# Kernel tuning notes

Hardware: AMD Instinct MI355X
Metric: run time of the kernel (lower is better)

Reference implementation:

```python
import jax, jax.numpy as jnp
import numpy as np

B, H, S, D = 1, 16, 4096, 64

def setup_inputs() -> dict:
    key = jax.random.key(0)
    k1, k2, k3 = jax.random.split(key, 3)
    query = jax.random.normal(k1, (B, H, S, D), dtype=jnp.float32)
    key_t = jax.random.normal(k2, (B, H, S, D), dtype=jnp.float32)
    value = jax.random.normal(k3, (B, H, S, D), dtype=jnp.float32)
    attn_mask = jnp.zeros((B, 1, S, S), dtype=jnp.float32)
    return {"query": query, "key": key_t, "value": value, "attn_mask": attn_mask}

def reference(query, key, value, attn_mask):
    d = query.shape[-1]
    # [B,H,S,S] = QK^T / sqrt(d) + mask
    scores = jnp.einsum("bhqd,bhkd->bhqk", query, key) / jnp.sqrt(jnp.float32(d))
    scores = scores + attn_mask
    probs = jax.nn.softmax(scores, axis=-1)
    # dropout_p = 0.0 -> identity
    out = jnp.einsum("bhqk,bhkd->bhqd", probs, value)
    return out
```

## Files before the change

kernel.cpp:

```cpp
#include <hip/hip_runtime.h>
#include <stdint.h>

#define LOG2E  1.44269504088896f
#define QSCALE (0.125f * LOG2E)

typedef float    f32x4_t  __attribute__((ext_vector_type(4)));
typedef float    f32x16_t __attribute__((ext_vector_type(16)));
typedef _Float16 f16x8_t  __attribute__((ext_vector_type(8)));
typedef _Float16 f16x2_t  __attribute__((ext_vector_type(2)));

#if __has_builtin(__builtin_amdgcn_exp2f)
#define EXP2F(x) __builtin_amdgcn_exp2f(x)
#else
#define EXP2F(x) exp2f(x)
#endif

__device__ __forceinline__ float rowsum2(f16x2_t p, float acc) {
#if __has_builtin(__builtin_amdgcn_fdot2)
  return __builtin_amdgcn_fdot2(p, (f16x2_t){(_Float16)1.0f, (_Float16)1.0f}, acc, false);
#else
  return acc + (float)p[0] + (float)p[1];
#endif
}

__global__ void mask_scan_kernel(const float* __restrict__ m, int* __restrict__ flag) {
  const float* p = m + (size_t)blockIdx.x * 8192 + (size_t)threadIdx.x * 4;
  unsigned acc = 0;
#pragma unroll
  for (int i = 0; i < 8; ++i) {
    f32x4_t v = *(const f32x4_t*)(p + (size_t)i * 1024);
    acc |= __float_as_uint(v[0]) | __float_as_uint(v[1]) |
           __float_as_uint(v[2]) | __float_as_uint(v[3]);
  }
  acc &= 0x7fffffffu;
  if (acc) atomicOr(flag, 1);
}

__global__ void convert_qk_kernel(const float* __restrict__ Q, const float* __restrict__ K,
                                  _Float16* __restrict__ Qh, _Float16* __restrict__ Kh) {
  const size_t idx = ((size_t)blockIdx.x * 256 + threadIdx.x) * 8;
  {
    f32x4_t a = *(const f32x4_t*)(Q + idx);
    f32x4_t b = *(const f32x4_t*)(Q + idx + 4);
    union { _Float16 h[8]; uint4 q; } U;
#pragma unroll
    for (int j = 0; j < 4; ++j) { U.h[j] = (_Float16)(a[j] * QSCALE); U.h[4 + j] = (_Float16)(b[j] * QSCALE); }
    *(uint4*)(Qh + idx) = U.q;
  }
  {
    f32x4_t a = *(const f32x4_t*)(K + idx);
    f32x4_t b = *(const f32x4_t*)(K + idx + 4);
    union { _Float16 h[8]; uint4 q; } U;
#pragma unroll
    for (int j = 0; j < 4; ++j) { U.h[j] = (_Float16)a[j]; U.h[4 + j] = (_Float16)b[j]; }
    *(uint4*)(Kh + idx) = U.q;
  }
}

__global__ void transpose_v_kernel(const float* __restrict__ V, _Float16* __restrict__ Vth) {
  __shared__ __align__(16) _Float16 T[64 * 72];
  const int tid  = threadIdx.x;
  const int head = blockIdx.x >> 6;
  const int st   = blockIdx.x & 63;
  const size_t hoff = (size_t)head * 4096 * 64;

  const int sl    = tid >> 2;
  const int fbase = (tid & 3) * 16;
  const float* src = V + hoff + (size_t)(st * 64 + sl) * 64 + fbase;
#pragma unroll
  for (int c = 0; c < 4; ++c) {
    f32x4_t a = *(const f32x4_t*)(src + c * 4);
#pragma unroll
    for (int j = 0; j < 4; ++j) T[(fbase + c * 4 + j) * 72 + sl] = (_Float16)a[j];
  }
  __syncthreads();
  const int feat = tid >> 2;
  const int sb   = (tid & 3) * 16;
  uint4 r0 = *(const uint4*)&T[feat * 72 + sb];
  uint4 r1 = *(const uint4*)&T[feat * 72 + sb + 8];
  _Float16* dst = Vth + hoff + (size_t)feat * 4096 + st * 64 + sb;
  *(uint4*)(dst)     = r0;
  *(uint4*)(dst + 8) = r1;
}

template <bool WS16>
__launch_bounds__(256, 2)
__global__ void sdpa_kernel(const float* __restrict__ Qg, const float* __restrict__ Kg,
                            const float* __restrict__ Vg, const float* __restrict__ Mg,
                            const _Float16* __restrict__ Qh, const _Float16* __restrict__ Kh,
                            const _Float16* __restrict__ Vth,
                            float* __restrict__ Og, const int* __restrict__ flag) {
  __shared__ __align__(16) _Float16 Ks[64 * 72];
  __shared__ __align__(16) _Float16 Vt[64 * 72];

  const int tid  = threadIdx.x;
  const int bid  = blockIdx.x;
  const int hh   = ((bid & 7) << 1) | ((bid >> 3) & 1);
  const int qt   = bid >> 4;
  const int w    = tid >> 6;
  const int lane = tid & 63;
  const int n    = lane & 31;
  const int h2   = lane >> 5;
  const int sig  = (n & 0x13) | ((n >> 1) & 4) | ((n << 1) & 8);
  const bool has_mask = (*flag) != 0;

  const size_t hoff = (size_t)hh * 4096 * 64;
  const int qcol = qt * 128 + w * 32 + n;

  f16x8_t qf[4];
  if (WS16) {
    const _Float16* qp = Qh + hoff + (size_t)qcol * 64 + 8 * h2;
#pragma unroll
    for (int kh = 0; kh < 4; ++kh) qf[kh] = *(const f16x8_t*)(qp + kh * 16);
  } else {
    const float* qp = Qg + hoff + (size_t)qcol * 64 + 8 * h2;
#pragma unroll
    for (int kh = 0; kh < 4; ++kh) {
      f32x4_t a = *(const f32x4_t*)(qp + kh * 16);
      f32x4_t b = *(const f32x4_t*)(qp + kh * 16 + 4);
      union { _Float16 h[8]; f16x8_t v; } U;
#pragma unroll
      for (int j = 0; j < 4; ++j) { U.h[j] = (_Float16)(a[j] * QSCALE); U.h[4 + j] = (_Float16)(b[j] * QSCALE); }
      qf[kh] = U.v;
    }
  }

  f32x16_t o0 = {0.f,0.f,0.f,0.f,0.f,0.f,0.f,0.f,0.f,0.f,0.f,0.f,0.f,0.f,0.f,0.f};
  f32x16_t o1 = o0;
  float lacc = 0.0f;

#pragma unroll 1
  for (int kt = 0; kt < 64; ++kt) {
    const int kbase = kt * 64;

    uint4 kk0, kk1, vv0, vv1;
    f32x4_t k0, k1, k2, k3;
    float vlo[8], vhi[8];
    if (WS16) {
      const _Float16* kp = Kh + hoff + (size_t)(kbase + (tid >> 2)) * 64 + (tid & 3) * 16;
      kk0 = *(const uint4*)(kp);
      kk1 = *(const uint4*)(kp + 8);
      const _Float16* vp = Vth + hoff + (size_t)(tid >> 2) * 4096 + kbase + (tid & 3) * 16;
      vv0 = *(const uint4*)(vp);
      vv1 = *(const uint4*)(vp + 8);
    } else {
      const float* kp = Kg + hoff + (size_t)(kbase + (tid >> 2)) * 64 + (tid & 3) * 16;
      k0 = *(const f32x4_t*)(kp + 0);
      k1 = *(const f32x4_t*)(kp + 4);
      k2 = *(const f32x4_t*)(kp + 8);
      k3 = *(const f32x4_t*)(kp + 12);
      const float* vp = Vg + hoff + (size_t)(kbase + (tid >> 5) * 8) * 64 + (tid & 31);
#pragma unroll
      for (int j = 0; j < 8; ++j) {
        vlo[j] = vp[(size_t)j * 64];
        vhi[j] = vp[(size_t)j * 64 + 32];
      }
    }

    f32x4_t mk[2][2][2];
    if (has_mask) {
      const float* mp = Mg + (size_t)qcol * 4096 + kbase + 8 * h2;
#pragma unroll
      for (int kb = 0; kb < 2; ++kb)
#pragma unroll
        for (int a = 0; a < 2; ++a)
#pragma unroll
          for (int b = 0; b < 2; ++b)
            mk[kb][a][b] = *(const f32x4_t*)(mp + kb * 32 + 16 * a + 4 * b);
    }

    __syncthreads();

    if (WS16) {
      *(uint4*)&Ks[(tid >> 2) * 72 + (tid & 3) * 16]     = kk0;
      *(uint4*)&Ks[(tid >> 2) * 72 + (tid & 3) * 16 + 8] = kk1;
      *(uint4*)&Vt[(tid >> 2) * 72 + (tid & 3) * 16]     = vv0;
      *(uint4*)&Vt[(tid >> 2) * 72 + (tid & 3) * 16 + 8] = vv1;
    } else {
      union { _Float16 h[8]; uint4 q; } A, B;
#pragma unroll
      for (int j = 0; j < 4; ++j) {
        A.h[j] = (_Float16)k0[j];  A.h[4 + j] = (_Float16)k1[j];
        B.h[j] = (_Float16)k2[j];  B.h[4 + j] = (_Float16)k3[j];
      }
      *(uint4*)&Ks[(tid >> 2) * 72 + (tid & 3) * 16]     = A.q;
      *(uint4*)&Ks[(tid >> 2) * 72 + (tid & 3) * 16 + 8] = B.q;
      union { _Float16 h[8]; uint4 q; } C, D;
#pragma unroll
      for (int j = 0; j < 8; ++j) { C.h[j] = (_Float16)vlo[j]; D.h[j] = (_Float16)vhi[j]; }
      *(uint4*)&Vt[(tid & 31) * 72 + (tid >> 5) * 8]        = C.q;
      *(uint4*)&Vt[((tid & 31) + 32) * 72 + (tid >> 5) * 8] = D.q;
    }

    __syncthreads();

#pragma unroll
    for (int kb = 0; kb < 2; ++kb) {
      f32x16_t acc = {0.f,0.f,0.f,0.f,0.f,0.f,0.f,0.f,0.f,0.f,0.f,0.f,0.f,0.f,0.f,0.f};
#pragma unroll
      for (int kh = 0; kh < 4; ++kh) {
        const f16x8_t ka = *(const f16x8_t*)&Ks[(kb * 32 + sig) * 72 + kh * 16 + 8 * h2];
        acc = __builtin_amdgcn_mfma_f32_32x32x16_f16(ka, qf[kh], acc, 0, 0, 0);
      }
#pragma unroll
      for (int a = 0; a < 2; ++a) {
        union { _Float16 h[8]; f16x8_t v; f16x2_t p2[4]; } F;
#pragma unroll
        for (int idx = 0; idx < 8; ++idx) {
          float x = acc[8 * a + idx];
          if (has_mask) x = __builtin_fmaf(mk[kb][a][idx >> 2][idx & 3], LOG2E, x);
          F.h[idx] = (_Float16)EXP2F(x);
        }
#pragma unroll
        for (int t = 0; t < 4; ++t) lacc = rowsum2(F.p2[t], lacc);
        const int f = kb * 2 + a;
        const f16x8_t v0 = *(const f16x8_t*)&Vt[n * 72 + f * 16 + 8 * h2];
        o0 = __builtin_amdgcn_mfma_f32_32x32x16_f16(F.v, v0, o0, 0, 0, 0);
        const f16x8_t v1 = *(const f16x8_t*)&Vt[(32 + n) * 72 + f * 16 + 8 * h2];
        o1 = __builtin_amdgcn_mfma_f32_32x32x16_f16(F.v, v1, o1, 0, 0, 0);
      }
    }
  }

  float lq = lacc + __shfl_xor(lacc, 32);
  float* op = Og + hoff;
#pragma unroll
  for (int r2 = 0; r2 < 4; ++r2) {
#pragma unroll
    for (int rr = 0; rr < 4; ++rr) {
      const int reg  = r2 * 4 + rr;
      const int qrow = rr + 8 * r2 + 4 * h2;
      float lr  = __shfl(lq, qrow);
      float inv = 1.0f / lr;
      const size_t row = (size_t)(qt * 128 + w * 32 + qrow) * 64;
      op[row + n]      = o0[reg] * inv;
      op[row + 32 + n] = o1[reg] * inv;
    }
  }
}

extern "C" void kernel_launch(void* const* d_in, const int* in_sizes, int n_in,
                              void* d_out, int out_size, void* d_ws, size_t ws_size,
                              hipStream_t stream) {
  const float* Q = (const float*)d_in[0];
  const float* K = (const float*)d_in[1];
  const float* V = (const float*)d_in[2];
  const float* M = (const float*)d_in[3];
  float* O = (float*)d_out;

  const size_t NELEM = (size_t)16 * 4096 * 64;
  const size_t need  = 256 + 3 * NELEM * sizeof(_Float16);
  int* flag = (int*)d_ws;

  hipMemsetAsync(flag, 0, sizeof(int), stream);
  mask_scan_kernel<<<2048, 256, 0, stream>>>(M, flag);

  if (ws_size >= need) {
    _Float16* Qh  = (_Float16*)((char*)d_ws + 256);
    _Float16* Kh  = Qh + NELEM;
    _Float16* Vth = Kh + NELEM;
    convert_qk_kernel<<<2048, 256, 0, stream>>>(Q, K, Qh, Kh);
    transpose_v_kernel<<<1024, 256, 0, stream>>>(V, Vth);
    sdpa_kernel<true><<<512, 256, 0, stream>>>(Q, K, V, M, Qh, Kh, Vth, O, flag);
  } else {
    sdpa_kernel<false><<<512, 256, 0, stream>>>(Q, K, V, M, nullptr, nullptr, nullptr, O, flag);
  }
}
```

Baseline: 234.3 us.

## Process 64 query rows per wave and prefetch next K/V tile in registers

```diff
diff --git a/kernel.cpp b/kernel.cpp
--- a/kernel.cpp
+++ b/kernel.cpp
@@ -83,13 +83,156 @@
   *(uint4*)(dst + 8) = r1;
 }
 
-template <bool WS16>
+__launch_bounds__(128, 2)
+__global__ void sdpa_kernel2(const _Float16* __restrict__ Qh, const _Float16* __restrict__ Kh,
+                             const _Float16* __restrict__ Vth, const float* __restrict__ Mg,
+                             float* __restrict__ Og, const int* __restrict__ flag) {
+  __shared__ __align__(16) _Float16 Ks[64 * 72];
+  __shared__ __align__(16) _Float16 Vt[64 * 72];
+
+  const int t    = threadIdx.x;
+  const int bid  = blockIdx.x;
+  const int hh   = ((bid & 7) << 1) | ((bid >> 3) & 1);
+  const int qt   = bid >> 4;
+  const int w    = t >> 6;
+  const int lane = t & 63;
+  const int n    = lane & 31;
+  const int h2   = lane >> 5;
+  const int sig  = (n & 0x13) | ((n >> 1) & 4) | ((n << 1) & 8);
+  const bool has_mask = (*flag) != 0;
+
+  const size_t hoff = (size_t)hh * 4096 * 64;
+  const int qb = qt * 128 + w * 64;
+
+  f16x8_t qf[2][4];
+#pragma unroll
+  for (int qh = 0; qh < 2; ++qh) {
+    const _Float16* qp = Qh + hoff + (size_t)(qb + qh * 32 + n) * 64 + 8 * h2;
+#pragma unroll
+    for (int kh = 0; kh < 4; ++kh) qf[qh][kh] = *(const f16x8_t*)(qp + kh * 16);
+  }
+
+  f32x16_t o00 = {0.f,0.f,0.f,0.f,0.f,0.f,0.f,0.f,0.f,0.f,0.f,0.f,0.f,0.f,0.f,0.f};
+  f32x16_t o01 = o00, o10 = o00, o11 = o00;
+  float lacc0 = 0.0f, lacc1 = 0.0f;
+
+  const int sr = t >> 1;
+  const int sh = (t & 1) * 32;
+  const _Float16* kbase_p = Kh  + hoff + (size_t)sr * 64 + sh;
+  const _Float16* vbase_p = Vth + hoff + (size_t)sr * 4096 + sh;
+
+  uint4 kk[4], vv[4];
+#pragma unroll
+  for (int j = 0; j < 4; ++j) {
+    kk[j] = ((const uint4*)kbase_p)[j];
+    vv[j] = ((const uint4*)vbase_p)[j];
+  }
+
+#pragma unroll 1
+  for (int kt = 0; kt < 64; ++kt) {
+    const int kbase = kt * 64;
+
+    __syncthreads();
+    {
+      uint4* kd = (uint4*)&Ks[sr * 72 + sh];
+      uint4* vd = (uint4*)&Vt[sr * 72 + sh];
+#pragma unroll
+      for (int j = 0; j < 4; ++j) { kd[j] = kk[j]; vd[j] = vv[j]; }
+    }
+    __syncthreads();
+
+    if (kt < 63) {
+      const _Float16* kp = kbase_p + (size_t)(kbase + 64) * 64;
+      const _Float16* vp = vbase_p + (kbase + 64);
+#pragma unroll
+      for (int j = 0; j < 4; ++j) {
+        kk[j] = ((const uint4*)kp)[j];
+        vv[j] = ((const uint4*)vp)[j];
+      }
+    }
+
+#pragma unroll
+    for (int kb = 0; kb < 2; ++kb) {
+      f16x8_t ka[4];
+#pragma unroll
+      for (int kh = 0; kh < 4; ++kh)
+        ka[kh] = *(const f16x8_t*)&Ks[(kb * 32 + sig) * 72 + kh * 16 + 8 * h2];
+      f32x16_t s0 = {0.f,0.f,0.f,0.f,0.f,0.f,0.f,0.f,0.f,0.f,0.f,0.f,0.f,0.f,0.f,0.f};
+      f32x16_t s1 = s0;
+#pragma unroll
+      for (int kh = 0; kh < 4; ++kh) {
+        s0 = __builtin_amdgcn_mfma_f32_32x32x16_f16(ka[kh], qf[0][kh], s0, 0, 0, 0);
+        s1 = __builtin_amdgcn_mfma_f32_32x32x16_f16(ka[kh], qf[1][kh], s1, 0, 0, 0);
+      }
+
+#pragma unroll
+      for (int a = 0; a < 2; ++a) {
+        const int f = kb * 2 + a;
+        const f16x8_t v0 = *(const f16x8_t*)&Vt[n * 72 + f * 16 + 8 * h2];
+        const f16x8_t v1 = *(const f16x8_t*)&Vt[(32 + n) * 72 + f * 16 + 8 * h2];
+#pragma unroll
+        for (int qh = 0; qh < 2; ++qh) {
+          union { _Float16 h[8]; f16x8_t v; f16x2_t p2[4]; } F;
+          f32x4_t m0, m1;
+          if (has_mask) {
+            const float* mp = Mg + (size_t)(qb + qh * 32 + n) * 4096 + kbase + kb * 32 + 16 * a + 8 * h2;
+            m0 = *(const f32x4_t*)(mp);
+            m1 = *(const f32x4_t*)(mp + 4);
+          }
+#pragma unroll
+          for (int idx = 0; idx < 8; ++idx) {
+            float x = (qh == 0) ? s0[8 * a + idx] : s1[8 * a + idx];
+            if (has_mask) {
+              float m = (idx < 4) ? m0[idx] : m1[idx - 4];
+              x = __builtin_fmaf(m, LOG2E, x);
+            }
+            F.h[idx] = (_Float16)EXP2F(x);
+          }
+          float* lp = (qh == 0) ? &lacc0 : &lacc1;
+#pragma unroll
+          for (int u = 0; u < 4; ++u) *lp = rowsum2(F.p2[u], *lp);
+          if (qh == 0) {
+            o00 = __builtin_amdgcn_mfma_f32_32x32x16_f16(F.v, v0, o00, 0, 0, 0);
+            o01 = __builtin_amdgcn_mfma_f32_32x32x16_f16(F.v, v1, o01, 0, 0, 0);
+          } else {
+            o10 = __builtin_amdgcn_mfma_f32_32x32x16_f16(F.v, v0, o10, 0, 0, 0);
+            o11 = __builtin_amdgcn_mfma_f32_32x32x16_f16(F.v, v1, o11, 0, 0, 0);
+          }
+        }
+      }
+    }
+  }
+
+  float* op = Og + hoff;
+#pragma unroll
+  for (int qh = 0; qh < 2; ++qh) {
+    float la = (qh == 0) ? lacc0 : lacc1;
+    float lq = la + __shfl_xor(la, 32);
+#pragma unroll
+    for (int r2 = 0; r2 < 4; ++r2) {
+#pragma unroll
+      for (int rr = 0; rr < 4; ++rr) {
+        const int reg  = r2 * 4 + rr;
+        const int qrow = rr + 8 * r2 + 4 * h2;
+        float lr  = __shfl(lq, qrow);
+        float inv = 1.0f / lr;
+        const size_t row = (size_t)(qb + qh * 32 + qrow) * 64;
+        if (qh == 0) {
+          op[row + n]      = o00[reg] * inv;
+          op[row + 32 + n] = o01[reg] * inv;
+        } else {
+          op[row + n]      = o10[reg] * inv;
+          op[row + 32 + n] = o11[reg] * inv;
+        }
+      }
+    }
+  }
+}
+
 __launch_bounds__(256, 2)
-__global__ void sdpa_kernel(const float* __restrict__ Qg, const float* __restrict__ Kg,
-                            const float* __restrict__ Vg, const float* __restrict__ Mg,
-                            const _Float16* __restrict__ Qh, const _Float16* __restrict__ Kh,
-                            const _Float16* __restrict__ Vth,
-                            float* __restrict__ Og, const int* __restrict__ flag) {
+__global__ void sdpa_kernel_fb(const float* __restrict__ Qg, const float* __restrict__ Kg,
+                               const float* __restrict__ Vg, const float* __restrict__ Mg,
+                               float* __restrict__ Og, const int* __restrict__ flag) {
   __shared__ __align__(16) _Float16 Ks[64 * 72];
   __shared__ __align__(16) _Float16 Vt[64 * 72];
 
@@ -108,11 +251,7 @@
   const int qcol = qt * 128 + w * 32 + n;
 
   f16x8_t qf[4];
-  if (WS16) {
-    const _Float16* qp = Qh + hoff + (size_t)qcol * 64 + 8 * h2;
-#pragma unroll
-    for (int kh = 0; kh < 4; ++kh) qf[kh] = *(const f16x8_t*)(qp + kh * 16);
-  } else {
+  {
     const float* qp = Qg + hoff + (size_t)qcol * 64 + 8 * h2;
 #pragma unroll
     for (int kh = 0; kh < 4; ++kh) {
@@ -132,30 +271,15 @@
 #pragma unroll 1
   for (int kt = 0; kt < 64; ++kt) {
     const int kbase = kt * 64;
-
-    uint4 kk0, kk1, vv0, vv1;
-    f32x4_t k0, k1, k2, k3;
+    const float* kp = Kg + hoff + (size_t)(kbase + (tid >> 2)) * 64 + (tid & 3) * 16;
+    f32x4_t k0 = *(const f32x4_t*)(kp + 0);
+    f32x4_t k1 = *(const f32x4_t*)(kp + 4);
+    f32x4_t k2 = *(const f32x4_t*)(kp + 8);
+    f32x4_t k3 = *(const f32x4_t*)(kp + 12);
+    const float* vp = Vg + hoff + (size_t)(kbase + (tid >> 5) * 8) * 64 + (tid & 31);
     float vlo[8], vhi[8];
-    if (WS16) {
-      const _Float16* kp = Kh + hoff + (size_t)(kbase + (tid >> 2)) * 64 + (tid & 3) * 16;
-      kk0 = *(const uint4*)(kp);
-      kk1 = *(const uint4*)(kp + 8);
-      const _Float16* vp = Vth + hoff + (size_t)(tid >> 2) * 4096 + kbase + (tid & 3) * 16;
-      vv0 = *(const uint4*)(vp);
-      vv1 = *(const uint4*)(vp + 8);
-    } else {
-      const float* kp = Kg + hoff + (size_t)(kbase + (tid >> 2)) * 64 + (tid & 3) * 16;
-      k0 = *(const f32x4_t*)(kp + 0);
-      k1 = *(const f32x4_t*)(kp + 4);
-      k2 = *(const f32x4_t*)(kp + 8);
-      k3 = *(const f32x4_t*)(kp + 12);
-      const float* vp = Vg + hoff + (size_t)(kbase + (tid >> 5) * 8) * 64 + (tid & 31);
-#pragma unroll
-      for (int j = 0; j < 8; ++j) {
-        vlo[j] = vp[(size_t)j * 64];
-        vhi[j] = vp[(size_t)j * 64 + 32];
-      }
-    }
+#pragma unroll
+    for (int j = 0; j < 8; ++j) { vlo[j] = vp[(size_t)j * 64]; vhi[j] = vp[(size_t)j * 64 + 32]; }
 
     f32x4_t mk[2][2][2];
     if (has_mask) {
@@ -170,13 +294,7 @@
     }
 
     __syncthreads();
-
-    if (WS16) {
-      *(uint4*)&Ks[(tid >> 2) * 72 + (tid & 3) * 16]     = kk0;
-      *(uint4*)&Ks[(tid >> 2) * 72 + (tid & 3) * 16 + 8] = kk1;
-      *(uint4*)&Vt[(tid >> 2) * 72 + (tid & 3) * 16]     = vv0;
-      *(uint4*)&Vt[(tid >> 2) * 72 + (tid & 3) * 16 + 8] = vv1;
-    } else {
+    {
       union { _Float16 h[8]; uint4 q; } A, B;
 #pragma unroll
       for (int j = 0; j < 4; ++j) {
@@ -191,7 +309,6 @@
       *(uint4*)&Vt[(tid & 31) * 72 + (tid >> 5) * 8]        = C.q;
       *(uint4*)&Vt[((tid & 31) + 32) * 72 + (tid >> 5) * 8] = D.q;
     }
-
     __syncthreads();
 
 #pragma unroll
@@ -212,7 +329,7 @@
           F.h[idx] = (_Float16)EXP2F(x);
         }
 #pragma unroll
-        for (int t = 0; t < 4; ++t) lacc = rowsum2(F.p2[t], lacc);
+        for (int u = 0; u < 4; ++u) lacc = rowsum2(F.p2[u], lacc);
         const int f = kb * 2 + a;
         const f16x8_t v0 = *(const f16x8_t*)&Vt[n * 72 + f * 16 + 8 * h2];
         o0 = __builtin_amdgcn_mfma_f32_32x32x16_f16(F.v, v0, o0, 0, 0, 0);
@@ -261,8 +378,8 @@
     _Float16* Vth = Kh + NELEM;
     convert_qk_kernel<<<2048, 256, 0, stream>>>(Q, K, Qh, Kh);
     transpose_v_kernel<<<1024, 256, 0, stream>>>(V, Vth);
-    sdpa_kernel<true><<<512, 256, 0, stream>>>(Q, K, V, M, Qh, Kh, Vth, O, flag);
+    sdpa_kernel2<<<512, 128, 0, stream>>>(Qh, Kh, Vth, M, O, flag);
   } else {
-    sdpa_kernel<false><<<512, 256, 0, stream>>>(Q, K, V, M, nullptr, nullptr, nullptr, O, flag);
-  }
-}
+    sdpa_kernel_fb<<<512, 256, 0, stream>>>(Q, K, V, M, O, flag);
+  }
+}
```

Result: slower. 333.0 us (+42.1%).
